# Kernel tuning notes

Hardware: AMD Instinct MI355X
Metric: run time of the kernel (lower is better)

## Reference

```python
import jax, jax.numpy as jnp
import numpy as np

D_STATE = 512


def _compute_ssm_matrices(S, K_raw, log_gamma, d_state):
    # K = K_raw / (sigma_max(K_raw).clamp(1e-5) + 0.002)  -- hard contraction
    sigma = jnp.linalg.norm(K_raw, ord=2)  # largest singular value
    sigma = jnp.maximum(sigma, 1e-5)
    K = K_raw / (sigma + 0.002)
    K11 = K[:d_state, :d_state]
    K12 = K[:d_state, d_state:]
    K21 = K[d_state:, :d_state]
    K22 = K[d_state:, d_state:]
    gamma = jnp.exp(log_gamma)
    Sinv = jnp.linalg.inv(S)
    A = Sinv @ K11 @ S
    B = gamma * (Sinv @ K12)
    C = K21 @ S
    D = gamma * K22
    return A, B, C, D


def setup_inputs() -> dict:
    key = jax.random.key(0)
    k1, k2, k3 = jax.random.split(key, 3)
    B_sz, T, H, N, P = 16, 4096, 512, 512, 512
    u = jax.random.normal(k1, (B_sz, T, H), dtype=jnp.float32)
    state = jnp.zeros((B_sz, N), dtype=jnp.float32)
    # S initialized as I + 0.01*randn (matches init_orthogonal_spectrum)
    S = jnp.eye(N, dtype=jnp.float32) + 0.01 * jax.random.normal(k2, (N, N), dtype=jnp.float32)
    K_raw = jax.random.normal(k3, (N + P, N + H), dtype=jnp.float32)
    log_gamma = jnp.zeros((), dtype=jnp.float32)  # gamma = 1.0
    return {"u": u, "state": state, "S": S, "K_raw": K_raw, "log_gamma": log_gamma}


def reference(u, state, S, K_raw, log_gamma):
    # u: [B,T,H], state: [B,N]
    A, Bm, C, D = _compute_ssm_matrices(S, K_raw, log_gamma, D_STATE)
    AT, BT, CT, DT = A.T, Bm.T, C.T, D.T

    def step(x, u_t):
        x_new = x @ AT + u_t @ BT  # [B,N]
        return x_new, x_new

    u_tbh = jnp.swapaxes(u, 0, 1)  # [T,B,H]
    _, xs = jax.lax.scan(step, state, u_tbh)  # xs: [T,B,N] = x_1..x_T
    states = jnp.concatenate([state[:, None, :], jnp.swapaxes(xs, 0, 1)], axis=1)  # [B,T+1,N]
    pre_states = states[:, :-1, :]  # x_0..x_{T-1}
    output = pre_states @ CT + u @ DT  # [B,T,d_output]
    return output, states
```

## Files before the change

kernel.cpp:

```cpp
#include <hip/hip_runtime.h>


typedef unsigned short u16;
typedef __bf16 bf16x8 __attribute__((ext_vector_type(8)));
typedef u16    u16x8  __attribute__((ext_vector_type(8)));
typedef float  f32x4  __attribute__((ext_vector_type(4)));

static_assert(sizeof(long) == 8, "need 64-bit long");

__device__ inline u16 f2bf(float f) {
    union { float f; unsigned u; } x; x.f = f;
    unsigned r = x.u + 0x7FFFu + ((x.u >> 16) & 1u);
    return (u16)(r >> 16);
}

__device__ inline bf16x8 cvt8(float4 v0, float4 v1) {
    bf16x8 a;
    a[0] = (__bf16)v0.x; a[1] = (__bf16)v0.y; a[2] = (__bf16)v0.z; a[3] = (__bf16)v0.w;
    a[4] = (__bf16)v1.x; a[5] = (__bf16)v1.y; a[6] = (__bf16)v1.z; a[7] = (__bf16)v1.w;
    return a;
}

__device__ inline void gl2lds16(const void* g, void* l) {
    auto gp = reinterpret_cast<const __attribute__((address_space(1))) char*>(
        (unsigned long long)g);
    auto lp = reinterpret_cast<__attribute__((address_space(3))) char*>(
        (unsigned)(unsigned long long)l);
    __builtin_amdgcn_global_load_lds(gp, lp, 16, 0, 0);
}

struct SArgs {
    const float* A1; long a1BS, a1RS; int a1Shift; unsigned a1Mask; int shiftA;
    int predLow; unsigned predMask;
    const float* A2; long a2BS, a2RS; int a2Shift; unsigned a2Mask;
    const u16* B1; const u16* B2;
    int K1c, Kc;
    const float* initP; float beta;
    float* Out; long oBS, oRS; int oShift; unsigned oMask;
    int sMode;
};

template<int MF>
__global__ __launch_bounds__(512, 4) void gemm_staged(SArgs g) {
    __shared__ char bstg[2][32768];
    const int tid = threadIdx.x, lane = tid & 63, wv = tid >> 6;
    const int kg = lane >> 4, l15 = lane & 15;
    const int rgw = wv >> 2, cg = wv & 3;
    const long row0 = (long)blockIdx.x * (32 * MF) + rgw * (16 * MF);
    const int cb = cg * 128;

    int Kc = g.Kc;
    const u16* B1 = g.B1;
    const u16* B2 = g.B2;
    float* Out = g.Out;
    if (g.sMode) {
        int s = blockIdx.z + 1;
        Kc = g.K1c + 16 * s;
        B1 = g.B1 + (long)(s - 1) * 262144;
        B2 = g.B2 + (long)(4 - s) * 262144;
        Out = g.Out + (long)s * 512;
    }
    const int K1c = g.K1c;

    const float* ap1[MF]; const float* ap2[MF]; bool pr[MF];
#pragma unroll
    for (int mf = 0; mf < MF; ++mf) {
        unsigned r = (unsigned)(row0 + mf * 16 + l15);
        pr[mf] = (g.predLow == 0) || ((r & g.predMask) >= (unsigned)g.predLow);
        long ra = (long)r - g.shiftA; if (ra < 0) ra = 0;
        ap1[mf] = g.A1 + ((ra >> g.a1Shift) * g.a1BS) + ((ra & (long)g.a1Mask) * g.a1RS) + kg * 8;
        ap2[mf] = nullptr;
        if (g.A2)
            ap2[mf] = g.A2 + (((long)(r >> g.a2Shift)) * g.a2BS) + ((long)(r & g.a2Mask) * g.a2RS) + kg * 8;
    }

    f32x4 acc[MF][8];
    if (g.initP) {
#pragma unroll
        for (int mf = 0; mf < MF; ++mf)
#pragma unroll
            for (int q = 0; q < 4; ++q) {
                unsigned r = (unsigned)(row0 + mf * 16 + kg * 4 + q);
                const float* ip = g.initP + ((long)(r >> g.oShift)) * g.oBS
                                + ((long)(r & g.oMask)) * g.oRS + cb + l15;
#pragma unroll
                for (int nf = 0; nf < 8; ++nf)
                    acc[mf][nf][q] = g.beta * ip[nf * 16];
            }
    } else {
#pragma unroll
        for (int mf = 0; mf < MF; ++mf)
#pragma unroll
            for (int nf = 0; nf < 8; ++nf)
                acc[mf][nf] = (f32x4){0.f, 0.f, 0.f, 0.f};
    }

    auto stage = [&](int c) {
        const char* src = (const char*)((c < K1c) ? (B1 + (long)c * 16384)
                                                  : (B2 + (long)(c - K1c) * 16384));
        char* dst = bstg[c & 1];
        const int wo = wv << 12;
#pragma unroll
        for (int i = 0; i < 4; ++i)
            gl2lds16(src + wo + (i << 10) + (lane << 4), dst + wo + (i << 10));
    };

    stage(0);
    if (Kc > 1) stage(1);
    __syncthreads();

    for (int c = 0; c < Kc; ++c) {
        bf16x8 af[MF];
        if (c < K1c) {
#pragma unroll
            for (int mf = 0; mf < MF; ++mf) {
                float4 v0 = *(const float4*)(ap1[mf]);
                float4 v1 = *(const float4*)(ap1[mf] + 4);
                ap1[mf] += 32;
                bf16x8 a = cvt8(v0, v1);
                if (!pr[mf]) { u16x8 z = {0,0,0,0,0,0,0,0}; a = __builtin_bit_cast(bf16x8, z); }
                af[mf] = a;
            }
        } else {
#pragma unroll
            for (int mf = 0; mf < MF; ++mf) {
                float4 v0 = *(const float4*)(ap2[mf]);
                float4 v1 = *(const float4*)(ap2[mf] + 4);
                ap2[mf] += 32;
                af[mf] = cvt8(v0, v1);
            }
        }
        const char* bb = bstg[c & 1] + kg * 8192 + (cb + l15) * 16;
#pragma unroll
        for (int nf = 0; nf < 8; ++nf) {
            u16x8 br = *(const u16x8*)(bb + nf * 256);
            bf16x8 bv = __builtin_bit_cast(bf16x8, br);
#pragma unroll
            for (int mf = 0; mf < MF; ++mf)
                acc[mf][nf] = __builtin_amdgcn_mfma_f32_16x16x32_bf16(af[mf], bv, acc[mf][nf], 0, 0, 0);
        }
        __syncthreads();
        if (c + 2 < Kc) stage(c + 2);
    }

#pragma unroll
    for (int mf = 0; mf < MF; ++mf)
#pragma unroll
        for (int q = 0; q < 4; ++q) {
            unsigned r = (unsigned)(row0 + mf * 16 + kg * 4 + q);
            float* op = Out + ((long)(r >> g.oShift)) * g.oBS
                      + ((long)(r & g.oMask)) * g.oRS + cb + l15;
#pragma unroll
            for (int nf = 0; nf < 8; ++nf) op[nf * 16] = acc[mf][nf][q];
        }
}

struct GemmArgs {
    const float* A1; long a1RS; int shiftA;
    const u16*   Bp; long ldbN, colOff;
    const float* initP; long iRS; float beta;
    float* Out; long oRS;
    int Kit; int predLow;
    float* sumsq;
    const float* scalePtr; float cScale;
    u16* OutP; long opLd;
};

__global__ __launch_bounds__(256) void gemm_bf16(GemmArgs g) {
    const int lane = threadIdx.x & 63;
    const int wv   = threadIdx.x >> 6;
    const int kg   = lane >> 4;
    const int l15  = lane & 15;
    const unsigned row0 = blockIdx.x * 16;
    const long cb = (long)blockIdx.y * 512 + wv * 128;

    unsigned rA = row0 + l15;
    bool pr = (g.predLow == 0) || (rA >= (unsigned)g.predLow);
    long ra = (long)rA - g.shiftA; if (ra < 0) ra = 0;
    const float* ap = g.A1 + ra * g.a1RS + kg * 8;

    f32x4 acc[8];
#pragma unroll
    for (int nf = 0; nf < 8; ++nf) acc[nf] = (f32x4){0.f, 0.f, 0.f, 0.f};

    if (g.initP) {
#pragma unroll
        for (int q = 0; q < 4; ++q) {
            unsigned r = row0 + kg * 4 + q;
            const float* ip = g.initP + (long)r * g.iRS + cb + l15;
#pragma unroll
            for (int nf = 0; nf < 8; ++nf) acc[nf][q] = g.beta * ip[nf * 16];
        }
    }

    const u16* bp = g.Bp + ((long)kg * g.ldbN + g.colOff + cb + l15) * 8;
    const long bstep = g.ldbN * 32;

    for (int kk = 0; kk < g.Kit; ++kk) {
        float4 v0 = *(const float4*)(ap);
        float4 v1 = *(const float4*)(ap + 4);
        ap += 32;
        bf16x8 a = cvt8(v0, v1);
        if (!pr) { u16x8 z = {0,0,0,0,0,0,0,0}; a = __builtin_bit_cast(bf16x8, z); }
#pragma unroll
        for (int nf = 0; nf < 8; ++nf) {
            u16x8 braw = *(const u16x8*)(bp + (long)nf * 128);
            bf16x8 bb = __builtin_bit_cast(bf16x8, braw);
            acc[nf] = __builtin_amdgcn_mfma_f32_16x16x32_bf16(a, bb, acc[nf], 0, 0, 0);
        }
        bp += bstep;
    }

    float sc = g.cScale;
    if (g.scalePtr) sc *= 1.0f / g.scalePtr[0];
    float ss = 0.f;
#pragma unroll
    for (int q = 0; q < 4; ++q) {
        unsigned r = row0 + kg * 4 + q;
        float* op = g.Out + (long)r * g.oRS + cb + l15;
#pragma unroll
        for (int nf = 0; nf < 8; ++nf) {
            float v = sc * acc[nf][q];
            op[nf * 16] = v;
            ss += v * v;
            if (g.OutP) {
                long col = cb + l15 + nf * 16;
                g.OutP[((long)(r >> 3) * g.opLd + col) * 8 + (r & 7)] = f2bf(v);
            }
        }
    }
    if (g.sumsq) {
#pragma unroll
        for (int off = 32; off; off >>= 1) ss += __shfl_down(ss, off);
        if (lane == 0) atomicAdd(g.sumsq, ss);
    }
}

__global__ __launch_bounds__(256) void gemm_f32_512(const float* A, const float* B,
                                                    const float* I, float* O,
                                                    float alpha, float beta) {
    __shared__ float As[16][68];
    __shared__ float Bs[16][68];
    const int tx = threadIdx.x & 15, ty = threadIdx.x >> 4;
    const int bm = blockIdx.x * 64, bn = blockIdx.y * 64;
    float acc[4][4] = {};
    for (int k0 = 0; k0 < 512; k0 += 16) {
        for (int t = threadIdx.x; t < 1024; t += 256) {
            int r = t >> 4, c = t & 15;
            As[c][r] = A[(long)(bm + r) * 512 + k0 + c];
            int r2 = t >> 6, c2 = t & 63;
            Bs[r2][c2] = B[(long)(k0 + r2) * 512 + bn + c2];
        }
        __syncthreads();
#pragma unroll
        for (int k = 0; k < 16; ++k)
#pragma unroll
            for (int i = 0; i < 4; ++i)
#pragma unroll
                for (int j = 0; j < 4; ++j)
                    acc[i][j] += As[k][ty * 4 + i] * Bs[k][tx * 4 + j];
        __syncthreads();
    }
#pragma unroll
    for (int i = 0; i < 4; ++i)
#pragma unroll
        for (int j = 0; j < 4; ++j) {
            long o = (long)(bm + ty * 4 + i) * 512 + bn + tx * 4 + j;
            float v = alpha * acc[i][j];
            if (I) v += beta * I[o];
            O[o] = v;
        }
}

__global__ __launch_bounds__(256) void k_cast_panel(const float* src, long srcLd, long R, long C,
                                                    u16* panel, long pLd) {
    long total = R * C;
    for (long idx = (long)blockIdx.x * 256 + threadIdx.x; idx < total; idx += (long)gridDim.x * 256) {
        long k = idx / C, n = idx % C;
        panel[((k >> 3) * pLd + n) * 8 + (k & 7)] = f2bf(src[k * srcLd + n]);
    }
}

__global__ __launch_bounds__(256) void k_transpose_cast(const float* src, long srcLd, long R, long C,
                                                        u16* panel, long pLd, float* dstFT,
                                                        const float* slots, int sIdx) {
    float scale = (sIdx >= 0) ? slots[sIdx] : 1.0f;
    long total = R * C;
    for (long idx = (long)blockIdx.x * 256 + threadIdx.x; idx < total; idx += (long)gridDim.x * 256) {
        long i = idx / C, j = idx % C;
        float v = src[i * srcLd + j] * scale;
        if (panel) panel[((j >> 3) * pLd + i) * 8 + (j & 7)] = f2bf(v);
        if (dstFT) dstFT[j * R + i] = v;
    }
}

__global__ __launch_bounds__(256) void k_x1(const float* S, float* Xf, u16* Xp) {
    for (long idx = (long)blockIdx.x * 256 + threadIdx.x; idx < 262144; idx += (long)gridDim.x * 256) {
        int i = (int)(idx >> 9), j = (int)(idx & 511);
        float v = ((i == j) ? 2.0f : 0.0f) - S[idx];
        Xf[idx] = v;
        Xp[(((long)(i >> 3)) * 512 + j) * 8 + (i & 7)] = f2bf(v);
    }
}

__global__ void k_fin(float* slots, const float* lg) {
    float lnacc = 0.f, w = 1.f;
    for (int i = 0; i <= 8; ++i) {
        lnacc += w * 0.5f * logf(fmaxf(slots[i], 1e-30f));
        w *= 0.5f;
    }
    float sigma = fmaxf(expf(0.5f * lnacc), 1e-5f);
    float s = sigma + 0.002f;
    slots[32] = 1.0f / s;
    slots[33] = expf(lg[0]) / s;
}

__global__ __launch_bounds__(256) void k_state0(float* states, const float* state) {
    int i = blockIdx.x * 256 + threadIdx.x;
    if (i < 8192) {
        int b = i >> 9, n = i & 511;
        states[(long)b * 2097664 + n] = state[i];
    }
}

__global__ __launch_bounds__(256) void k_xc(float* Xc, const float* Zb, const float* state) {
    long total = 16384L * 128;
    for (long i = (long)blockIdx.x * 256 + threadIdx.x; i < total; i += (long)gridDim.x * 256) {
        long r = i >> 7; int o = (int)(i & 127);
        long c = r & 1023;
        float4 v;
        if (c == 0) v = *(const float4*)(state + (r >> 10) * 512 + o * 4);
        else        v = *(const float4*)(Zb + (r - 1) * 512 + o * 4);
        *(float4*)(Xc + r * 512 + o * 4) = v;
    }
}

extern "C" void kernel_launch(void* const* d_in, const int* in_sizes, int n_in,
                              void* d_out, int out_size, void* d_ws, size_t ws_size,
                              hipStream_t stream) {
    (void)in_sizes; (void)n_in; (void)out_size; (void)ws_size;

    const float* u     = (const float*)d_in[0];
    const float* state = (const float*)d_in[1];
    const float* S     = (const float*)d_in[2];
    const float* K     = (const float*)d_in[3];
    const float* lg    = (const float*)d_in[4];

    float* out    = (float*)d_out;
    float* states = out + 33554432L;
    float* Zb     = out;
    float* Xc     = out + 8388608L;

    char* w = (char*)d_ws;
    auto alloc = [&](size_t n) { void* p = w; w += (n + 255) & ~(size_t)255; return p; };
    float* slots = (float*)alloc(256);
    u16* Qall = (u16*)alloc(4L * 262144 * 2);
    u16* W4p  = (u16*)alloc(4L * 262144 * 2);
    u16* Q8p  = (u16*)alloc(262144L * 2);
    u16* Q16p = (u16*)alloc(262144L * 2);
    u16* CDT  = (u16*)alloc(2L * 262144 * 2);
    float* Qf   = (float*)alloc(4L * 262144 * 4);
    float* W4f  = (float*)alloc(4L * 262144 * 4);
    float* Q8f  = (float*)alloc(262144L * 4);
    float* Q16f = (float*)alloc(262144L * 4);
    float* Za   = (float*)w;
    float* KTf = (float*)alloc(1024L * 1024 * 4);
    u16*   Kp  = (u16*)  alloc(1024L * 1024 * 2);
    float* Mf  = (float*)alloc(1024L * 1024 * 4);
    u16*   Mp  = (u16*)  alloc(1024L * 1024 * 2);
    float* Mf2 = (float*)alloc(1024L * 1024 * 4);
    u16*   Mp2 = (u16*)  alloc(1024L * 1024 * 2);
    u16*   Sp  = (u16*)  alloc(512L * 512 * 2);
    float* Xaf = (float*)alloc(512L * 512 * 4);
    u16*   Xap = (u16*)  alloc(512L * 512 * 2);
    float* Xbf = (float*)alloc(512L * 512 * 4);
    u16*   Xbp = (u16*)  alloc(512L * 512 * 2);
    float* Pf  = (float*)alloc(512L * 512 * 4);
    u16*   Pp  = (u16*)  alloc(512L * 512 * 2);
    float* Xs  = (float*)alloc(512L * 512 * 4);
    float* T1f = (float*)alloc(512L * 512 * 4);
    u16*   T1p = (u16*)  alloc(512L * 512 * 2);
    float* Af  = (float*)alloc(512L * 512 * 4);
    float* Bmf = (float*)alloc(512L * 512 * 4);
    float* Cmf = (float*)alloc(512L * 512 * 4);

    auto mkargs = [&]() { GemmArgs a = {}; a.beta = 1.f; a.cScale = 1.f; return a; };
    auto launch_gemm = [&](int M, int N, const GemmArgs& a) {
        dim3 gr(M / 16, N / 512);
        gemm_bf16<<<gr, 256, 0, stream>>>(a);
    };

    hipMemsetAsync(slots, 0, 256, stream);

    k_transpose_cast<<<4096, 256, 0, stream>>>(K, 1024, 1024, 1024, nullptr, 0, KTf, nullptr, -1);
    k_cast_panel<<<4096, 256, 0, stream>>>(K, 1024, 1024, 1024, Kp, 1024);
    {   GemmArgs a = mkargs();
        a.A1 = KTf; a.a1RS = 1024;
        a.Bp = Kp; a.ldbN = 1024;
        a.Out = Mf; a.oRS = 1024; a.OutP = Mp; a.opLd = 1024;
        a.Kit = 32; a.sumsq = slots + 0;
        launch_gemm(1024, 1024, a);
    }
    {   float* Fs[2] = {Mf, Mf2};
        u16*   Ps[2] = {Mp, Mp2};
        for (int i = 1; i <= 8; ++i) {
            GemmArgs a = mkargs();
            a.A1 = Fs[(i + 1) & 1]; a.a1RS = 1024;
            a.Bp = Ps[(i + 1) & 1]; a.ldbN = 1024;
            a.Out = Fs[i & 1]; a.oRS = 1024; a.OutP = Ps[i & 1]; a.opLd = 1024;
            a.Kit = 32; a.sumsq = slots + i; a.scalePtr = slots + (i - 1);
            launch_gemm(1024, 1024, a);
        }
    }
    k_fin<<<1, 1, 0, stream>>>(slots, lg);

    k_cast_panel<<<1024, 256, 0, stream>>>(S, 512, 512, 512, Sp, 512);
    k_x1<<<1024, 256, 0, stream>>>(S, Xaf, Xap);
    float* curF = Xaf; u16* curP = Xap; float* nxtF = Xbf; u16* nxtP = Xbp;
    for (int it = 0; it < 4; ++it) {
        GemmArgs a = mkargs();
        a.A1 = S; a.a1RS = 512;
        a.Bp = curP; a.ldbN = 512;
        a.Out = Pf; a.oRS = 512; a.OutP = Pp; a.opLd = 512; a.cScale = -1.f;
        a.Kit = 16;
        launch_gemm(512, 512, a);
        GemmArgs b = mkargs();
        b.A1 = curF; b.a1RS = 512;
        b.Bp = Pp; b.ldbN = 512;
        b.initP = curF; b.iRS = 512; b.beta = 2.f;
        b.Out = nxtF; b.oRS = 512; b.OutP = nxtP; b.opLd = 512;
        b.Kit = 16;
        launch_gemm(512, 512, b);
        float* tf = curF; curF = nxtF; nxtF = tf;
        u16*   tp = curP; curP = nxtP; nxtP = tp;
    }
    gemm_f32_512<<<dim3(8, 8), 256, 0, stream>>>(S, curF, nullptr, Pf, 1.f, 0.f);
    gemm_f32_512<<<dim3(8, 8), 256, 0, stream>>>(curF, Pf, curF, Xs, -1.f, 2.f);

    {   GemmArgs a = mkargs();
        a.A1 = K; a.a1RS = 1024; a.Bp = Sp; a.ldbN = 512;
        a.Out = T1f; a.oRS = 512; a.OutP = T1p; a.opLd = 512; a.Kit = 16;
        launch_gemm(512, 512, a);
    }
    {   GemmArgs a = mkargs();
        a.A1 = Xs; a.a1RS = 512; a.Bp = T1p; a.ldbN = 512;
        a.Out = Af; a.oRS = 512; a.Kit = 16;
        launch_gemm(512, 512, a);
    }
    {   GemmArgs a = mkargs();
        a.A1 = Xs; a.a1RS = 512; a.Bp = Kp; a.ldbN = 1024; a.colOff = 512;
        a.Out = Bmf; a.oRS = 512; a.Kit = 16;
        launch_gemm(512, 512, a);
    }
    {   GemmArgs a = mkargs();
        a.A1 = K + 512L * 1024; a.a1RS = 1024; a.Bp = Sp; a.ldbN = 512;
        a.Out = Cmf; a.oRS = 512; a.Kit = 16;
        launch_gemm(512, 512, a);
    }
    k_transpose_cast<<<1024, 256, 0, stream>>>(Af, 512, 512, 512, Qall, 512, Qf, slots, 32);
    k_transpose_cast<<<1024, 256, 0, stream>>>(Bmf, 512, 512, 512, W4p + 3 * 262144, 512,
                                               W4f + 3 * 262144, slots, 33);
    k_transpose_cast<<<1024, 256, 0, stream>>>(Cmf, 512, 512, 512, CDT, 512, nullptr, slots, 32);
    k_transpose_cast<<<1024, 256, 0, stream>>>(K + 512L * 1024 + 512, 1024, 512, 512,
                                               CDT + 262144, 512, nullptr, slots, 33);
    {   GemmArgs a = mkargs();
        a.A1 = Qf; a.a1RS = 512; a.Bp = Qall; a.ldbN = 512;
        a.Out = Qf + 262144; a.oRS = 512; a.OutP = Qall + 262144; a.opLd = 512; a.Kit = 16;
        launch_gemm(512, 512, a);
        a.A1 = Qf; a.Bp = Qall + 262144;
        a.Out = Qf + 2 * 262144; a.OutP = Qall + 2 * 262144;
        launch_gemm(1024, 512, a);
        a.A1 = Qf + 3 * 262144; a.Bp = Qall + 3 * 262144;
        a.Out = Q8f; a.OutP = Q8p;
        launch_gemm(512, 512, a);
        a.A1 = Q8f; a.Bp = Q8p;
        a.Out = Q16f; a.OutP = Q16p;
        launch_gemm(512, 512, a);
    }
    {   GemmArgs a = mkargs();
        a.A1 = W4f + 3 * 262144; a.a1RS = 512; a.Bp = Qall; a.ldbN = 512;
        a.Out = W4f + 2 * 262144; a.oRS = 512; a.OutP = W4p + 2 * 262144; a.opLd = 512; a.Kit = 16;
        launch_gemm(512, 512, a);
        a.A1 = W4f + 2 * 262144; a.Bp = Qall + 262144;
        a.Out = W4f; a.OutP = W4p;
        launch_gemm(1024, 512, a);
    }

    {   SArgs a = {};
        a.A1 = u; a.a1BS = 2097152; a.a1RS = 2048; a.a1Shift = 10; a.a1Mask = 1023;
        a.predMask = 1023;
        a.B1 = W4p; a.B2 = W4p; a.K1c = 64; a.Kc = 64;
        a.beta = 1.f;
        a.Out = Za; a.oBS = 0; a.oRS = 512; a.oShift = 14; a.oMask = 16383;
        gemm_staged<1><<<dim3(512, 1, 1), 512, 0, stream>>>(a);
    }
    {   GemmArgs f = mkargs();
        f.A1 = state; f.a1RS = 512;
        f.Bp = Qall + 3 * 262144; f.ldbN = 512;
        f.initP = Za; f.iRS = 524288; f.beta = 1.f;
        f.Out = Za; f.oRS = 524288; f.Kit = 16;
        launch_gemm(16, 512, f);
    }
    auto ks = [&](const float* src, float* dst, int d, const u16* gen) {
        SArgs a = {};
        a.A1 = src; a.a1BS = 0; a.a1RS = 512; a.a1Shift = 14; a.a1Mask = 16383;
        a.shiftA = d; a.predLow = d; a.predMask = 1023;
        a.B1 = gen; a.B2 = gen; a.K1c = 16; a.Kc = 16;
        a.initP = src; a.beta = 1.f;
        a.Out = dst; a.oBS = 0; a.oRS = 512; a.oShift = 14; a.oMask = 16383;
        gemm_staged<1><<<dim3(512, 1, 1), 512, 0, stream>>>(a);
    };
    ks(Za, Zb, 1, Qall + 3 * 262144);
    ks(Zb, Za, 2, Q8p);
    ks(Za, Zb, 4, Q16p);

    k_xc<<<2048, 256, 0, stream>>>(Xc, Zb, state);
    k_state0<<<32, 256, 0, stream>>>(states, state);
    {   SArgs a = {};
        a.A1 = Xc; a.a1BS = 0; a.a1RS = 512; a.a1Shift = 14; a.a1Mask = 16383;
        a.predMask = 1023;
        a.A2 = u; a.a2BS = 2097152; a.a2RS = 2048; a.a2Shift = 10; a.a2Mask = 1023;
        a.B1 = Qall; a.B2 = W4p; a.K1c = 16; a.Kc = 0;
        a.beta = 1.f;
        a.Out = states; a.oBS = 2097664; a.oRS = 2048; a.oShift = 10; a.oMask = 1023;
        a.sMode = 1;
        gemm_staged<2><<<dim3(256, 1, 4), 512, 0, stream>>>(a);
    }

    {   SArgs a = {};
        a.A1 = states; a.a1BS = 2097664; a.a1RS = 512; a.a1Shift = 12; a.a1Mask = 4095;
        a.predMask = 4095;
        a.A2 = u; a.a2BS = 2097152; a.a2RS = 512; a.a2Shift = 12; a.a2Mask = 4095;
        a.B1 = CDT; a.B2 = CDT + 262144; a.K1c = 16; a.Kc = 32;
        a.beta = 1.f;
        a.Out = out; a.oBS = 2097152; a.oRS = 512; a.oShift = 12; a.oMask = 4095;
        gemm_staged<2><<<dim3(1024, 1, 1), 512, 0, stream>>>(a);
    }
}
```

Baseline: 1.324 ms.

## Prefetch A tiles, fuse transposes, drop Xc copy, cut Newton iteration

```diff
diff --git a/kernel.cpp b/kernel.cpp
--- a/kernel.cpp
+++ b/kernel.cpp
@@ -35,7 +35,7 @@
     const float* A2; long a2BS, a2RS; int a2Shift; unsigned a2Mask;
     const u16* B1; const u16* B2;
     int K1c, Kc;
-    const float* initP; float beta;
+    const float* initP; long iBS, iRS; int iShift; unsigned iMask; float beta;
     float* Out; long oBS, oRS; int oShift; unsigned oMask;
     int sMode;
 };
@@ -81,8 +81,8 @@
 #pragma unroll
             for (int q = 0; q < 4; ++q) {
                 unsigned r = (unsigned)(row0 + mf * 16 + kg * 4 + q);
-                const float* ip = g.initP + ((long)(r >> g.oShift)) * g.oBS
-                                + ((long)(r & g.oMask)) * g.oRS + cb + l15;
+                const float* ip = g.initP + ((long)(r >> g.iShift)) * g.iBS
+                                + ((long)(r & g.iMask)) * g.iRS + cb + l15;
 #pragma unroll
                 for (int nf = 0; nf < 8; ++nf)
                     acc[mf][nf][q] = g.beta * ip[nf * 16];
@@ -105,31 +105,42 @@
             gl2lds16(src + wo + (i << 10) + (lane << 4), dst + wo + (i << 10));
     };
 
+    auto loadA = [&](int c, float4* v0, float4* v1) {
+        if (c < K1c) {
+#pragma unroll
+            for (int mf = 0; mf < MF; ++mf) {
+                v0[mf] = *(const float4*)(ap1[mf]);
+                v1[mf] = *(const float4*)(ap1[mf] + 4);
+                ap1[mf] += 32;
+            }
+        } else {
+#pragma unroll
+            for (int mf = 0; mf < MF; ++mf) {
+                v0[mf] = *(const float4*)(ap2[mf]);
+                v1[mf] = *(const float4*)(ap2[mf] + 4);
+                ap2[mf] += 32;
+            }
+        }
+    };
+
     stage(0);
     if (Kc > 1) stage(1);
+    float4 pv0[MF], pv1[MF];
+    loadA(0, pv0, pv1);
+    bool maskCur = (0 < K1c);
     __syncthreads();
 
     for (int c = 0; c < Kc; ++c) {
         bf16x8 af[MF];
-        if (c < K1c) {
-#pragma unroll
-            for (int mf = 0; mf < MF; ++mf) {
-                float4 v0 = *(const float4*)(ap1[mf]);
-                float4 v1 = *(const float4*)(ap1[mf] + 4);
-                ap1[mf] += 32;
-                bf16x8 a = cvt8(v0, v1);
-                if (!pr[mf]) { u16x8 z = {0,0,0,0,0,0,0,0}; a = __builtin_bit_cast(bf16x8, z); }
-                af[mf] = a;
-            }
-        } else {
-#pragma unroll
-            for (int mf = 0; mf < MF; ++mf) {
-                float4 v0 = *(const float4*)(ap2[mf]);
-                float4 v1 = *(const float4*)(ap2[mf] + 4);
-                ap2[mf] += 32;
-                af[mf] = cvt8(v0, v1);
-            }
-        }
+#pragma unroll
+        for (int mf = 0; mf < MF; ++mf) {
+            bf16x8 a = cvt8(pv0[mf], pv1[mf]);
+            if (maskCur && !pr[mf]) { u16x8 z = {0,0,0,0,0,0,0,0}; a = __builtin_bit_cast(bf16x8, z); }
+            af[mf] = a;
+        }
+        if (c + 1 < Kc) loadA(c + 1, pv0, pv1);
+        maskCur = (c + 1 < K1c);
+
         const char* bb = bstg[c & 1] + kg * 8192 + (cb + l15) * 16;
 #pragma unroll
         for (int nf = 0; nf < 8; ++nf) {
@@ -294,10 +305,36 @@
     }
 }
 
-__global__ __launch_bounds__(256) void k_x1(const float* S, float* Xf, u16* Xp) {
+struct T4Args {
+    const float* src0; const float* src1; const float* src2; const float* src3;
+    long ld0, ld1, ld2, ld3;
+    u16 *p0, *p1, *p2, *p3;
+    float *f0, *f1, *f2, *f3;
+    int s0, s1, s2, s3;
+    const float* slots;
+};
+__global__ __launch_bounds__(256) void k_transpose4(T4Args t) {
+    int m = blockIdx.y;
+    const float* src; long ld; u16* panel; float* dstFT; int sIdx;
+    if (m == 0) { src = t.src0; ld = t.ld0; panel = t.p0; dstFT = t.f0; sIdx = t.s0; }
+    else if (m == 1) { src = t.src1; ld = t.ld1; panel = t.p1; dstFT = t.f1; sIdx = t.s1; }
+    else if (m == 2) { src = t.src2; ld = t.ld2; panel = t.p2; dstFT = t.f2; sIdx = t.s2; }
+    else { src = t.src3; ld = t.ld3; panel = t.p3; dstFT = t.f3; sIdx = t.s3; }
+    float scale = (sIdx >= 0) ? t.slots[sIdx] : 1.0f;
+    for (long idx = (long)blockIdx.x * 256 + threadIdx.x; idx < 262144; idx += (long)gridDim.x * 256) {
+        long i = idx >> 9, j = idx & 511;
+        float v = src[i * ld + j] * scale;
+        panel[((j >> 3) * 512 + i) * 8 + (j & 7)] = f2bf(v);
+        if (dstFT) dstFT[j * 512 + i] = v;
+    }
+}
+
+__global__ __launch_bounds__(256) void k_sx1(const float* S, u16* Sp, float* Xf, u16* Xp) {
     for (long idx = (long)blockIdx.x * 256 + threadIdx.x; idx < 262144; idx += (long)gridDim.x * 256) {
         int i = (int)(idx >> 9), j = (int)(idx & 511);
-        float v = ((i == j) ? 2.0f : 0.0f) - S[idx];
+        float sv = S[idx];
+        Sp[(((long)(i >> 3)) * 512 + j) * 8 + (i & 7)] = f2bf(sv);
+        float v = ((i == j) ? 2.0f : 0.0f) - sv;
         Xf[idx] = v;
         Xp[(((long)(i >> 3)) * 512 + j) * 8 + (i & 7)] = f2bf(v);
     }
@@ -323,18 +360,6 @@
     }
 }
 
-__global__ __launch_bounds__(256) void k_xc(float* Xc, const float* Zb, const float* state) {
-    long total = 16384L * 128;
-    for (long i = (long)blockIdx.x * 256 + threadIdx.x; i < total; i += (long)gridDim.x * 256) {
-        long r = i >> 7; int o = (int)(i & 127);
-        long c = r & 1023;
-        float4 v;
-        if (c == 0) v = *(const float4*)(state + (r >> 10) * 512 + o * 4);
-        else        v = *(const float4*)(Zb + (r - 1) * 512 + o * 4);
-        *(float4*)(Xc + r * 512 + o * 4) = v;
-    }
-}
-
 extern "C" void kernel_launch(void* const* d_in, const int* in_sizes, int n_in,
                               void* d_out, int out_size, void* d_ws, size_t ws_size,
                               hipStream_t stream) {
@@ -349,7 +374,6 @@
     float* out    = (float*)d_out;
     float* states = out + 33554432L;
     float* Zb     = out;
-    float* Xc     = out + 8388608L;
 
     char* w = (char*)d_ws;
     auto alloc = [&](size_t n) { void* p = w; w += (n + 255) & ~(size_t)255; return p; };
@@ -414,10 +438,9 @@
     }
     k_fin<<<1, 1, 0, stream>>>(slots, lg);
 
-    k_cast_panel<<<1024, 256, 0, stream>>>(S, 512, 512, 512, Sp, 512);
-    k_x1<<<1024, 256, 0, stream>>>(S, Xaf, Xap);
+    k_sx1<<<1024, 256, 0, stream>>>(S, Sp, Xaf, Xap);
     float* curF = Xaf; u16* curP = Xap; float* nxtF = Xbf; u16* nxtP = Xbp;
-    for (int it = 0; it < 4; ++it) {
+    for (int it = 0; it < 3; ++it) {
         GemmArgs a = mkargs();
         a.A1 = S; a.a1RS = 512;
         a.Bp = curP; a.ldbN = 512;
@@ -457,12 +480,14 @@
         a.Out = Cmf; a.oRS = 512; a.Kit = 16;
         launch_gemm(512, 512, a);
     }
-    k_transpose_cast<<<1024, 256, 0, stream>>>(Af, 512, 512, 512, Qall, 512, Qf, slots, 32);
-    k_transpose_cast<<<1024, 256, 0, stream>>>(Bmf, 512, 512, 512, W4p + 3 * 262144, 512,
-                                               W4f + 3 * 262144, slots, 33);
-    k_transpose_cast<<<1024, 256, 0, stream>>>(Cmf, 512, 512, 512, CDT, 512, nullptr, slots, 32);
-    k_transpose_cast<<<1024, 256, 0, stream>>>(K + 512L * 1024 + 512, 1024, 512, 512,
-                                               CDT + 262144, 512, nullptr, slots, 33);
+    {   T4Args t = {};
+        t.src0 = Af;  t.ld0 = 512;  t.p0 = Qall;            t.f0 = Qf;            t.s0 = 32;
+        t.src1 = Bmf; t.ld1 = 512;  t.p1 = W4p + 3*262144;  t.f1 = W4f + 3*262144; t.s1 = 33;
+        t.src2 = Cmf; t.ld2 = 512;  t.p2 = CDT;             t.f2 = nullptr;       t.s2 = 32;
+        t.src3 = K + 512L*1024 + 512; t.ld3 = 1024; t.p3 = CDT + 262144; t.f3 = nullptr; t.s3 = 33;
+        t.slots = slots;
+        k_transpose4<<<dim3(512, 4), 256, 0, stream>>>(t);
+    }
     {   GemmArgs a = mkargs();
         a.A1 = Qf; a.a1RS = 512; a.Bp = Qall; a.ldbN = 512;
         a.Out = Qf + 262144; a.oRS = 512; a.OutP = Qall + 262144; a.opLd = 512; a.Kit = 16;
@@ -492,7 +517,7 @@
         a.B1 = W4p; a.B2 = W4p; a.K1c = 64; a.Kc = 64;
         a.beta = 1.f;
         a.Out = Za; a.oBS = 0; a.oRS = 512; a.oShift = 14; a.oMask = 16383;
-        gemm_staged<1><<<dim3(512, 1, 1), 512, 0, stream>>>(a);
+        gemm_staged<2><<<dim3(256, 1, 1), 512, 0, stream>>>(a);
     }
     {   GemmArgs f = mkargs();
         f.A1 = state; f.a1RS = 512;
@@ -501,30 +526,38 @@
         f.Out = Za; f.oRS = 524288; f.Kit = 16;
         launch_gemm(16, 512, f);
     }
+    k_state0<<<32, 256, 0, stream>>>(states, state);
+
     auto ks = [&](const float* src, float* dst, int d, const u16* gen) {
         SArgs a = {};
         a.A1 = src; a.a1BS = 0; a.a1RS = 512; a.a1Shift = 14; a.a1Mask = 16383;
         a.shiftA = d; a.predLow = d; a.predMask = 1023;
         a.B1 = gen; a.B2 = gen; a.K1c = 16; a.Kc = 16;
-        a.initP = src; a.beta = 1.f;
+        a.initP = src; a.iBS = 0; a.iRS = 512; a.iShift = 14; a.iMask = 16383; a.beta = 1.f;
         a.Out = dst; a.oBS = 0; a.oRS = 512; a.oShift = 14; a.oMask = 16383;
-        gemm_staged<1><<<dim3(512, 1, 1), 512, 0, stream>>>(a);
+        gemm_staged<2><<<dim3(256, 1, 1), 512, 0, stream>>>(a);
     };
     ks(Za, Zb, 1, Qall + 3 * 262144);
     ks(Zb, Za, 2, Q8p);
-    ks(Za, Zb, 4, Q16p);
-
-    k_xc<<<2048, 256, 0, stream>>>(Xc, Zb, state);
-    k_state0<<<32, 256, 0, stream>>>(states, state);
+    {
+        SArgs a = {};
+        a.A1 = Za; a.a1BS = 0; a.a1RS = 512; a.a1Shift = 14; a.a1Mask = 16383;
+        a.shiftA = 4; a.predLow = 4; a.predMask = 1023;
+        a.B1 = Q16p; a.B2 = Q16p; a.K1c = 16; a.Kc = 16;
+        a.initP = Za; a.iBS = 0; a.iRS = 512; a.iShift = 14; a.iMask = 16383; a.beta = 1.f;
+        a.Out = states + 2048; a.oBS = 2097664; a.oRS = 2048; a.oShift = 10; a.oMask = 1023;
+        gemm_staged<2><<<dim3(256, 1, 1), 512, 0, stream>>>(a);
+    }
+
     {   SArgs a = {};
-        a.A1 = Xc; a.a1BS = 0; a.a1RS = 512; a.a1Shift = 14; a.a1Mask = 16383;
+        a.A1 = states; a.a1BS = 2097664; a.a1RS = 2048; a.a1Shift = 10; a.a1Mask = 1023;
         a.predMask = 1023;
         a.A2 = u; a.a2BS = 2097152; a.a2RS = 2048; a.a2Shift = 10; a.a2Mask = 1023;
         a.B1 = Qall; a.B2 = W4p; a.K1c = 16; a.Kc = 0;
         a.beta = 1.f;
         a.Out = states; a.oBS = 2097664; a.oRS = 2048; a.oShift = 10; a.oMask = 1023;
         a.sMode = 1;
-        gemm_staged<2><<<dim3(256, 1, 4), 512, 0, stream>>>(a);
+        gemm_staged<2><<<dim3(256, 1, 3), 512, 0, stream>>>(a);
     }
 
     {   SArgs a = {};
```

After: 1.264 ms. 4.5% less time.
